# Kernel tuning notes

Hardware: AMD Instinct MI355X
Metric: run time of the kernel (lower is better)

## Reference

```python
import jax, jax.numpy as jnp
import numpy as np

HIDDEN = 128
AUG = 2          # aug_dim
SUBSTEPS = 2     # fixed dopri5 substeps per output interval (replaces adaptive stepping)
B = 16384
T = 8


def _xavier(key, shape, gain=5.0 / 3.0):
    fan_in, fan_out = shape
    lim = gain * np.sqrt(6.0 / (fan_in + fan_out))
    return jax.random.uniform(key, shape, jnp.float32, -lim, lim)


def setup_inputs() -> dict:
    key = jax.random.key(0)
    ks = jax.random.split(key, 4)
    return {
        "r0": jax.random.normal(ks[0], (B, 2), jnp.float32),
        "t": jnp.linspace(0.0, 1.0, T, dtype=jnp.float32),
        "W1": _xavier(ks[1], (5, HIDDEN)),
        "b1": jnp.zeros((HIDDEN,), jnp.float32),
        "W2": _xavier(ks[2], (HIDDEN, HIDDEN)),
        "b2": jnp.zeros((HIDDEN,), jnp.float32),
        "W3": _xavier(ks[3], (HIDDEN, 2)),
        "b3": jnp.zeros((2,), jnp.float32),
    }


def _ode_f(t, s, W1, b1, W2, b2, W3, b3):
    # s: [B, 2+AUG]; t: scalar -> concat time feature, tiny tanh MLP
    tf = t * jnp.ones((s.shape[0], 1), s.dtype)
    inp = jnp.concatenate([s, tf], axis=-1)            # [B, 5]
    h = jnp.tanh(inp @ W1 + b1)                        # [B, 128]
    h = jnp.tanh(h @ W2 + b2)                          # [B, 128]
    v_xy = h @ W3 + b3                                 # [B, 2]
    v_a = jnp.zeros((s.shape[0], AUG), s.dtype)        # static aug dynamics
    return jnp.concatenate([v_xy, v_a], axis=-1)


def _dopri5_step(f, t, s, dt):
    # Dormand-Prince RK45 tableau, 5th-order solution advance (as torchdiffeq dopri5)
    k1 = f(t, s)
    k2 = f(t + dt * (1.0 / 5.0), s + dt * (1.0 / 5.0) * k1)
    k3 = f(t + dt * (3.0 / 10.0), s + dt * ((3.0 / 40.0) * k1 + (9.0 / 40.0) * k2))
    k4 = f(t + dt * (4.0 / 5.0),
           s + dt * ((44.0 / 45.0) * k1 - (56.0 / 15.0) * k2 + (32.0 / 9.0) * k3))
    k5 = f(t + dt * (8.0 / 9.0),
           s + dt * ((19372.0 / 6561.0) * k1 - (25360.0 / 2187.0) * k2
                     + (64448.0 / 6561.0) * k3 - (212.0 / 729.0) * k4))
    k6 = f(t + dt,
           s + dt * ((9017.0 / 3168.0) * k1 - (355.0 / 33.0) * k2
                     + (46732.0 / 5247.0) * k3 + (49.0 / 176.0) * k4
                     - (5103.0 / 18656.0) * k5))
    return s + dt * ((35.0 / 384.0) * k1 + (500.0 / 1113.0) * k3
                     + (125.0 / 192.0) * k4 - (2187.0 / 6784.0) * k5
                     + (11.0 / 84.0) * k6)


def _integrate(r0, t, W1, b1, W2, b2, W3, b3):
    s0 = jnp.concatenate([r0, jnp.zeros((r0.shape[0], AUG), r0.dtype)], axis=-1)
    f = lambda tt, ss: _ode_f(tt, ss, W1, b1, W2, b2, W3, b3)

    def interval(s, ts):
        t0, t1 = ts
        dt = (t1 - t0) / SUBSTEPS
        for j in range(SUBSTEPS):  # small fixed loop, unrolled
            s = _dopri5_step(f, t0 + j * dt, s, dt)
        return s, s

    _, ys = jax.lax.scan(interval, s0, (t[:-1], t[1:]))   # [T-1, B, 4]
    traj = jnp.concatenate([s0[None], ys], axis=0)        # [T, B, 4]
    return jnp.transpose(traj, (1, 0, 2))[..., :2]        # [B, T, 2]


def reference(r0, t, W1, b1, W2, b2, W3, b3):
    return _integrate(r0, t, W1, b1, W2, b2, W3, b3)
```

## Files before the change

### kernel.cpp

```cpp
#include <hip/hip_runtime.h>


#define HID 128
#define NS  16
#define NWAVE 4
#define TT  8
#define F(a,b) ((float)((double)(a)/(double)(b)))

typedef __attribute__((ext_vector_type(8))) short bf16x8;
typedef __attribute__((ext_vector_type(4))) float f32x4;
typedef __attribute__((ext_vector_type(2))) float f32x2;

union Frag { bf16x8 v; unsigned short u[8]; unsigned int d[4]; };

__device__ __forceinline__ f32x2 bc(float s) { return f32x2{s, s}; }
__device__ __forceinline__ f32x2 pk_fma(f32x2 a, f32x2 b, f32x2 c) {
#if __has_builtin(__builtin_elementwise_fma)
  return __builtin_elementwise_fma(a, b, c);
#else
  return a * b + c;
#endif
}
__device__ __forceinline__ float exp2_fast(float x) {
#if __has_builtin(__builtin_amdgcn_exp2f)
  return __builtin_amdgcn_exp2f(x);
#else
  return __builtin_exp2f(x);
#endif
}

__device__ __forceinline__ unsigned short f2bf(float f) {
  unsigned u = __builtin_bit_cast(unsigned, f);
  u += 0x7FFFu + ((u >> 16) & 1u);
  return (unsigned short)(u >> 16);
}
__device__ __forceinline__ unsigned pack2bf(float a, float b) {
  unsigned ua = __builtin_bit_cast(unsigned, a);
  unsigned ub = __builtin_bit_cast(unsigned, b);
  ua += 0x7FFFu + ((ua >> 16) & 1u);
  ub += 0x7FFFu + ((ub >> 16) & 1u);
  return __builtin_amdgcn_perm(ub, ua, 0x07060302u);
}

__device__ __forceinline__ f32x2 tanh_pk(f32x2 x) {
  const float K2 = 2.8853900817779268f;
  f32x2 u = x * bc(K2);
  f32x2 e;
  e.x = exp2_fast(u.x);
  e.y = exp2_fast(u.y);
  f32x2 d = e + bc(1.0f);
  f32x2 r;
  r.x = __builtin_amdgcn_rcpf(d.x);
  r.y = __builtin_amdgcn_rcpf(d.y);
  return pk_fma(bc(-2.0f), r, bc(1.0f));
}

__global__ __launch_bounds__(256, 4) void node_kernel(
    const float* __restrict__ r0, const float* __restrict__ tarr,
    const float* __restrict__ W1, const float* __restrict__ b1,
    const float* __restrict__ W2, const float* __restrict__ b2,
    const float* __restrict__ W3, const float* __restrict__ b3,
    float* __restrict__ out)
{
  __shared__ uint4  h1L[16 * NS];
  __shared__ float2 vrS[NWAVE * NS];

  const int tid  = (int)threadIdx.x;
  const int lane = tid & 63;
  const int w    = __builtin_amdgcn_readfirstlane(tid >> 6);
  const int quad = lane >> 4;
  const int m16  = lane & 15;
  const int n    = tid & 15;
  const int r    = tid >> 4;
  const int s    = (int)blockIdx.x * NS + n;

  f32x2 w1x[4], w1y[4], w1t[4], bb1[4];
  #pragma unroll
  for (int p = 0; p < 4; ++p) {
    int i = r * 8 + 2 * p;
    w1x[p] = f32x2{W1[0 * HID + i], W1[0 * HID + i + 1]};
    w1y[p] = f32x2{W1[1 * HID + i], W1[1 * HID + i + 1]};
    w1t[p] = f32x2{W1[4 * HID + i], W1[4 * HID + i + 1]};
    bb1[p] = f32x2{b1[i], b1[i + 1]};
  }
  Frag Ah[2][4];
  #pragma unroll
  for (int oti = 0; oti < 2; ++oti) {
    int o = (2 * w + oti) * 16 + m16;
    #pragma unroll
    for (int kk = 0; kk < 4; ++kk)
      #pragma unroll
      for (int j = 0; j < 8; ++j)
        Ah[oti][kk].u[j] = f2bf(W2[(kk * 32 + quad * 8 + j) * HID + o]);
  }
  f32x2 b2p[2][2], w3xy[2][4];
  #pragma unroll
  for (int oti = 0; oti < 2; ++oti) {
    #pragma unroll
    for (int p = 0; p < 2; ++p) {
      int o = (2 * w + oti) * 16 + quad * 4 + 2 * p;
      b2p[oti][p] = f32x2{b2[o], b2[o + 1]};
    }
    #pragma unroll
    for (int rr = 0; rr < 4; ++rr) {
      int o = (2 * w + oti) * 16 + quad * 4 + rr;
      w3xy[oti][rr] = f32x2{W3[o * 2 + 0], W3[o * 2 + 1]};
    }
  }
  const f32x2 b3v = f32x2{b3[0], b3[1]};

  f32x2 S = f32x2{r0[2 * s + 0], r0[2 * s + 1]};
  if (tid < NS) *(float2*)&out[(s * TT + 0) * 2] = make_float2(S.x, S.y);

  auto feval = [&](float tt, f32x2 st) -> f32x2 {
    const f32x2 sx = bc(st.x), sy = bc(st.y), tv = bc(tt);
    {
      uint4 pk;
      unsigned pd[4];
      #pragma unroll
      for (int p = 0; p < 4; ++p) {
        f32x2 a = pk_fma(sx, w1x[p], bb1[p]);
        a = pk_fma(sy, w1y[p], a);
        a = pk_fma(tv, w1t[p], a);
        f32x2 h = tanh_pk(a);
        pd[p] = pack2bf(h.x, h.y);
      }
      pk.x = pd[0]; pk.y = pd[1]; pk.z = pd[2]; pk.w = pd[3];
      h1L[r * NS + n] = pk;
    }
    __syncthreads();
    f32x4 acc[2];
    acc[0] = f32x4{0.f, 0.f, 0.f, 0.f};
    acc[1] = f32x4{0.f, 0.f, 0.f, 0.f};
    #pragma unroll
    for (int kk = 0; kk < 4; ++kk) {
      Frag bfr;
      uint4 t4 = h1L[(kk * 4 + quad) * NS + m16];
      bfr.d[0] = t4.x; bfr.d[1] = t4.y; bfr.d[2] = t4.z; bfr.d[3] = t4.w;
      acc[0] = __builtin_amdgcn_mfma_f32_16x16x32_bf16(Ah[0][kk].v, bfr.v, acc[0], 0, 0, 0);
      acc[1] = __builtin_amdgcn_mfma_f32_16x16x32_bf16(Ah[1][kk].v, bfr.v, acc[1], 0, 0, 0);
    }
    f32x2 vsum = bc(0.f);
    #pragma unroll
    for (int oti = 0; oti < 2; ++oti) {
      #pragma unroll
      for (int p = 0; p < 2; ++p) {
        f32x2 av = f32x2{acc[oti][2 * p], acc[oti][2 * p + 1]} + b2p[oti][p];
        f32x2 h2 = tanh_pk(av);
        vsum = pk_fma(bc(h2.x), w3xy[oti][2 * p + 0], vsum);
        vsum = pk_fma(bc(h2.y), w3xy[oti][2 * p + 1], vsum);
      }
    }
    float px = vsum.x, py = vsum.y;
    px += __shfl_xor(px, 16); px += __shfl_xor(px, 32);
    py += __shfl_xor(py, 16); py += __shfl_xor(py, 32);
    if (lane < 16) vrS[w * NS + m16] = make_float2(px, py);
    __syncthreads();
    f32x2 rv = b3v;
    #pragma unroll
    for (int ww = 0; ww < NWAVE; ++ww) {
      float2 pp = vrS[ww * NS + n];
      rv += f32x2{pp.x, pp.y};
    }
    return rv;
  };

  #pragma unroll 1
  for (int iv = 0; iv < TT - 1; ++iv) {
    float t0 = tarr[iv], t1 = tarr[iv + 1];
    float dt = (t1 - t0) * 0.5f;
    #pragma unroll 1
    for (int ss = 0; ss < 2; ++ss) {
      float tb = (ss == 0) ? t0 : (t0 + dt);
      const f32x2 dtv = bc(dt);
      f32x2 k1 = feval(tb, S);
      f32x2 k2 = feval(tb + dt * F(1,5), pk_fma(bc(dt * F(1,5)), k1, S));
      f32x2 a3 = pk_fma(bc(F(9,40)), k2, bc(F(3,40)) * k1);
      f32x2 k3 = feval(tb + dt * F(3,10), pk_fma(dtv, a3, S));
      f32x2 a4 = pk_fma(bc(F(44,45)), k1,
                 pk_fma(bc(-F(56,15)), k2, bc(F(32,9)) * k3));
      f32x2 k4 = feval(tb + dt * F(4,5), pk_fma(dtv, a4, S));
      f32x2 a5 = pk_fma(bc(F(19372,6561)), k1,
                 pk_fma(bc(-F(25360,2187)), k2,
                 pk_fma(bc(F(64448,6561)), k3, bc(-F(212,729)) * k4)));
      f32x2 k5 = feval(tb + dt * F(8,9), pk_fma(dtv, a5, S));
      f32x2 a6 = pk_fma(bc(F(9017,3168)), k1,
                 pk_fma(bc(-F(355,33)), k2,
                 pk_fma(bc(F(46732,5247)), k3,
                 pk_fma(bc(F(49,176)), k4, bc(-F(5103,18656)) * k5))));
      f32x2 k6 = feval(tb + dt, pk_fma(dtv, a6, S));
      f32x2 fin = pk_fma(bc(F(35,384)), k1,
                  pk_fma(bc(F(500,1113)), k3,
                  pk_fma(bc(F(125,192)), k4,
                  pk_fma(bc(-F(2187,6784)), k5, bc(F(11,84)) * k6))));
      S = pk_fma(dtv, fin, S);
    }
    if (tid < NS) *(float2*)&out[(s * TT + iv + 1) * 2] = make_float2(S.x, S.y);
  }
}

extern "C" void kernel_launch(void* const* d_in, const int* in_sizes, int n_in,
                              void* d_out, int out_size, void* d_ws, size_t ws_size,
                              hipStream_t stream) {
  const float* r0 = (const float*)d_in[0];
  const float* t  = (const float*)d_in[1];
  const float* W1 = (const float*)d_in[2];
  const float* b1 = (const float*)d_in[3];
  const float* W2 = (const float*)d_in[4];
  const float* b2 = (const float*)d_in[5];
  const float* W3 = (const float*)d_in[6];
  const float* b3 = (const float*)d_in[7];
  float* out = (float*)d_out;
  const int B = in_sizes[0] / 2;
  dim3 grid(B / NS), block(NWAVE * 64);
  node_kernel<<<grid, block, 0, stream>>>(r0, t, W1, b1, W2, b2, W3, b3, out);
}
```

Measured before the change: 203.8 us.

## Process two sample groups per block and fold tanh scale into weights

```diff
diff --git a/kernel.cpp b/kernel.cpp
--- a/kernel.cpp
+++ b/kernel.cpp
@@ -2,7 +2,7 @@
 
 
 #define HID 128
-#define NS  16
+#define NSG 16
 #define NWAVE 4
 #define TT  8
 #define F(a,b) ((float)((double)(a)/(double)(b)))
@@ -28,7 +28,6 @@
   return __builtin_exp2f(x);
 #endif
 }
-
 __device__ __forceinline__ unsigned short f2bf(float f) {
   unsigned u = __builtin_bit_cast(unsigned, f);
   u += 0x7FFFu + ((u >> 16) & 1u);
@@ -41,10 +40,7 @@
   ub += 0x7FFFu + ((ub >> 16) & 1u);
   return __builtin_amdgcn_perm(ub, ua, 0x07060302u);
 }
-
-__device__ __forceinline__ f32x2 tanh_pk(f32x2 x) {
-  const float K2 = 2.8853900817779268f;
-  f32x2 u = x * bc(K2);
+__device__ __forceinline__ f32x2 tanh_pre(f32x2 u) {
   f32x2 e;
   e.x = exp2_fast(u.x);
   e.y = exp2_fast(u.y);
@@ -55,15 +51,17 @@
   return pk_fma(bc(-2.0f), r, bc(1.0f));
 }
 
-__global__ __launch_bounds__(256, 4) void node_kernel(
+#define K2C 2.8853900817779268f
+
+__global__ __launch_bounds__(256, 2) void node_kernel(
     const float* __restrict__ r0, const float* __restrict__ tarr,
     const float* __restrict__ W1, const float* __restrict__ b1,
     const float* __restrict__ W2, const float* __restrict__ b2,
     const float* __restrict__ W3, const float* __restrict__ b3,
     float* __restrict__ out)
 {
-  __shared__ uint4  h1L[16 * NS];
-  __shared__ float2 vrS[NWAVE * NS];
+  __shared__ uint4  h1L[2][16 * NSG];
+  __shared__ float2 vrS[2][NWAVE * NSG];
 
   const int tid  = (int)threadIdx.x;
   const int lane = tid & 63;
@@ -72,16 +70,17 @@
   const int m16  = lane & 15;
   const int n    = tid & 15;
   const int r    = tid >> 4;
-  const int s    = (int)blockIdx.x * NS + n;
+  const int sA   = (int)blockIdx.x * (2 * NSG) + n;
+  const int sB   = sA + NSG;
 
   f32x2 w1x[4], w1y[4], w1t[4], bb1[4];
   #pragma unroll
   for (int p = 0; p < 4; ++p) {
     int i = r * 8 + 2 * p;
-    w1x[p] = f32x2{W1[0 * HID + i], W1[0 * HID + i + 1]};
-    w1y[p] = f32x2{W1[1 * HID + i], W1[1 * HID + i + 1]};
-    w1t[p] = f32x2{W1[4 * HID + i], W1[4 * HID + i + 1]};
-    bb1[p] = f32x2{b1[i], b1[i + 1]};
+    w1x[p] = f32x2{W1[0 * HID + i], W1[0 * HID + i + 1]} * bc(K2C);
+    w1y[p] = f32x2{W1[1 * HID + i], W1[1 * HID + i + 1]} * bc(K2C);
+    w1t[p] = f32x2{W1[4 * HID + i], W1[4 * HID + i + 1]} * bc(K2C);
+    bb1[p] = f32x2{b1[i], b1[i + 1]} * bc(K2C);
   }
   Frag Ah[2][4];
   #pragma unroll
@@ -91,7 +90,7 @@
     for (int kk = 0; kk < 4; ++kk)
       #pragma unroll
       for (int j = 0; j < 8; ++j)
-        Ah[oti][kk].u[j] = f2bf(W2[(kk * 32 + quad * 8 + j) * HID + o]);
+        Ah[oti][kk].u[j] = f2bf(W2[(kk * 32 + quad * 8 + j) * HID + o] * K2C);
   }
   f32x2 b2p[2][2], w3xy[2][4];
   #pragma unroll
@@ -99,7 +98,7 @@
     #pragma unroll
     for (int p = 0; p < 2; ++p) {
       int o = (2 * w + oti) * 16 + quad * 4 + 2 * p;
-      b2p[oti][p] = f32x2{b2[o], b2[o + 1]};
+      b2p[oti][p] = f32x2{b2[o], b2[o + 1]} * bc(K2C);
     }
     #pragma unroll
     for (int rr = 0; rr < 4; ++rr) {
@@ -109,60 +108,92 @@
   }
   const f32x2 b3v = f32x2{b3[0], b3[1]};
 
-  f32x2 S = f32x2{r0[2 * s + 0], r0[2 * s + 1]};
-  if (tid < NS) *(float2*)&out[(s * TT + 0) * 2] = make_float2(S.x, S.y);
-
-  auto feval = [&](float tt, f32x2 st) -> f32x2 {
+  f32x2 SA = f32x2{r0[2 * sA + 0], r0[2 * sA + 1]};
+  f32x2 SB = f32x2{r0[2 * sB + 0], r0[2 * sB + 1]};
+  if (tid < 32) {
+    int g = tid >> 4;
+    int ss = (int)blockIdx.x * (2 * NSG) + tid;
+    f32x2 S0 = g ? SB : SA;
+    *(float2*)&out[(ss * TT + 0) * 2] = make_float2(S0.x, S0.y);
+  }
+
+  auto layer1 = [&](int g, f32x2 st, float tt) {
     const f32x2 sx = bc(st.x), sy = bc(st.y), tv = bc(tt);
-    {
-      uint4 pk;
-      unsigned pd[4];
-      #pragma unroll
-      for (int p = 0; p < 4; ++p) {
-        f32x2 a = pk_fma(sx, w1x[p], bb1[p]);
-        a = pk_fma(sy, w1y[p], a);
-        a = pk_fma(tv, w1t[p], a);
-        f32x2 h = tanh_pk(a);
-        pd[p] = pack2bf(h.x, h.y);
-      }
-      pk.x = pd[0]; pk.y = pd[1]; pk.z = pd[2]; pk.w = pd[3];
-      h1L[r * NS + n] = pk;
-    }
+    unsigned pd[4];
+    #pragma unroll
+    for (int p = 0; p < 4; ++p) {
+      f32x2 a = pk_fma(sx, w1x[p], bb1[p]);
+      a = pk_fma(sy, w1y[p], a);
+      a = pk_fma(tv, w1t[p], a);
+      f32x2 h = tanh_pre(a);
+      pd[p] = pack2bf(h.x, h.y);
+    }
+    h1L[g][r * NSG + n] = make_uint4(pd[0], pd[1], pd[2], pd[3]);
+  };
+
+  auto feval2 = [&](float tt, f32x2 stA, f32x2 stB, f32x2& vA, f32x2& vB) {
+    layer1(0, stA, tt);
+    layer1(1, stB, tt);
     __syncthreads();
-    f32x4 acc[2];
-    acc[0] = f32x4{0.f, 0.f, 0.f, 0.f};
-    acc[1] = f32x4{0.f, 0.f, 0.f, 0.f};
+    Frag bfA[4], bfB[4];
     #pragma unroll
     for (int kk = 0; kk < 4; ++kk) {
-      Frag bfr;
-      uint4 t4 = h1L[(kk * 4 + quad) * NS + m16];
-      bfr.d[0] = t4.x; bfr.d[1] = t4.y; bfr.d[2] = t4.z; bfr.d[3] = t4.w;
-      acc[0] = __builtin_amdgcn_mfma_f32_16x16x32_bf16(Ah[0][kk].v, bfr.v, acc[0], 0, 0, 0);
-      acc[1] = __builtin_amdgcn_mfma_f32_16x16x32_bf16(Ah[1][kk].v, bfr.v, acc[1], 0, 0, 0);
-    }
-    f32x2 vsum = bc(0.f);
-    #pragma unroll
-    for (int oti = 0; oti < 2; ++oti) {
+      uint4 ta = h1L[0][(kk * 4 + quad) * NSG + m16];
+      bfA[kk].d[0] = ta.x; bfA[kk].d[1] = ta.y; bfA[kk].d[2] = ta.z; bfA[kk].d[3] = ta.w;
+      uint4 tb = h1L[1][(kk * 4 + quad) * NSG + m16];
+      bfB[kk].d[0] = tb.x; bfB[kk].d[1] = tb.y; bfB[kk].d[2] = tb.z; bfB[kk].d[3] = tb.w;
+    }
+    f32x4 accA[2], accB[2];
+    accA[0] = f32x4{0.f,0.f,0.f,0.f}; accA[1] = f32x4{0.f,0.f,0.f,0.f};
+    accB[0] = f32x4{0.f,0.f,0.f,0.f}; accB[1] = f32x4{0.f,0.f,0.f,0.f};
+    #pragma unroll
+    for (int kk = 0; kk < 4; ++kk) {
+      accA[0] = __builtin_amdgcn_mfma_f32_16x16x32_bf16(Ah[0][kk].v, bfA[kk].v, accA[0], 0, 0, 0);
+      accA[1] = __builtin_amdgcn_mfma_f32_16x16x32_bf16(Ah[1][kk].v, bfA[kk].v, accA[1], 0, 0, 0);
+    }
+    #pragma unroll
+    for (int kk = 0; kk < 4; ++kk) {
+      accB[0] = __builtin_amdgcn_mfma_f32_16x16x32_bf16(Ah[0][kk].v, bfB[kk].v, accB[0], 0, 0, 0);
+      accB[1] = __builtin_amdgcn_mfma_f32_16x16x32_bf16(Ah[1][kk].v, bfB[kk].v, accB[1], 0, 0, 0);
+    }
+    f32x2 vsA = bc(0.f), vsB = bc(0.f);
+    #pragma unroll
+    for (int oti = 0; oti < 2; ++oti)
       #pragma unroll
       for (int p = 0; p < 2; ++p) {
-        f32x2 av = f32x2{acc[oti][2 * p], acc[oti][2 * p + 1]} + b2p[oti][p];
-        f32x2 h2 = tanh_pk(av);
-        vsum = pk_fma(bc(h2.x), w3xy[oti][2 * p + 0], vsum);
-        vsum = pk_fma(bc(h2.y), w3xy[oti][2 * p + 1], vsum);
-      }
-    }
-    float px = vsum.x, py = vsum.y;
-    px += __shfl_xor(px, 16); px += __shfl_xor(px, 32);
-    py += __shfl_xor(py, 16); py += __shfl_xor(py, 32);
-    if (lane < 16) vrS[w * NS + m16] = make_float2(px, py);
+        f32x2 av = f32x2{accA[oti][2*p], accA[oti][2*p+1]} + b2p[oti][p];
+        f32x2 h2 = tanh_pre(av);
+        vsA = pk_fma(bc(h2.x), w3xy[oti][2*p+0], vsA);
+        vsA = pk_fma(bc(h2.y), w3xy[oti][2*p+1], vsA);
+      }
+    #pragma unroll
+    for (int oti = 0; oti < 2; ++oti)
+      #pragma unroll
+      for (int p = 0; p < 2; ++p) {
+        f32x2 av = f32x2{accB[oti][2*p], accB[oti][2*p+1]} + b2p[oti][p];
+        f32x2 h2 = tanh_pre(av);
+        vsB = pk_fma(bc(h2.x), w3xy[oti][2*p+0], vsB);
+        vsB = pk_fma(bc(h2.y), w3xy[oti][2*p+1], vsB);
+      }
+    float pxA = vsA.x, pyA = vsA.y, pxB = vsB.x, pyB = vsB.y;
+    pxA += __shfl_xor(pxA, 16); pxA += __shfl_xor(pxA, 32);
+    pyA += __shfl_xor(pyA, 16); pyA += __shfl_xor(pyA, 32);
+    pxB += __shfl_xor(pxB, 16); pxB += __shfl_xor(pxB, 32);
+    pyB += __shfl_xor(pyB, 16); pyB += __shfl_xor(pyB, 32);
+    if (lane < 16) {
+      vrS[0][w * NSG + m16] = make_float2(pxA, pyA);
+      vrS[1][w * NSG + m16] = make_float2(pxB, pyB);
+    }
     __syncthreads();
-    f32x2 rv = b3v;
+    f32x2 ra = b3v, rb = b3v;
     #pragma unroll
     for (int ww = 0; ww < NWAVE; ++ww) {
-      float2 pp = vrS[ww * NS + n];
-      rv += f32x2{pp.x, pp.y};
-    }
-    return rv;
+      float2 pa = vrS[0][ww * NSG + n];
+      float2 pb = vrS[1][ww * NSG + n];
+      ra += f32x2{pa.x, pa.y};
+      rb += f32x2{pb.x, pb.y};
+    }
+    vA = ra; vB = rb;
   };
 
   #pragma unroll 1
@@ -173,29 +204,53 @@
     for (int ss = 0; ss < 2; ++ss) {
       float tb = (ss == 0) ? t0 : (t0 + dt);
       const f32x2 dtv = bc(dt);
-      f32x2 k1 = feval(tb, S);
-      f32x2 k2 = feval(tb + dt * F(1,5), pk_fma(bc(dt * F(1,5)), k1, S));
-      f32x2 a3 = pk_fma(bc(F(9,40)), k2, bc(F(3,40)) * k1);
-      f32x2 k3 = feval(tb + dt * F(3,10), pk_fma(dtv, a3, S));
-      f32x2 a4 = pk_fma(bc(F(44,45)), k1,
-                 pk_fma(bc(-F(56,15)), k2, bc(F(32,9)) * k3));
-      f32x2 k4 = feval(tb + dt * F(4,5), pk_fma(dtv, a4, S));
-      f32x2 a5 = pk_fma(bc(F(19372,6561)), k1,
-                 pk_fma(bc(-F(25360,2187)), k2,
-                 pk_fma(bc(F(64448,6561)), k3, bc(-F(212,729)) * k4)));
-      f32x2 k5 = feval(tb + dt * F(8,9), pk_fma(dtv, a5, S));
-      f32x2 a6 = pk_fma(bc(F(9017,3168)), k1,
-                 pk_fma(bc(-F(355,33)), k2,
-                 pk_fma(bc(F(46732,5247)), k3,
-                 pk_fma(bc(F(49,176)), k4, bc(-F(5103,18656)) * k5))));
-      f32x2 k6 = feval(tb + dt, pk_fma(dtv, a6, S));
-      f32x2 fin = pk_fma(bc(F(35,384)), k1,
-                  pk_fma(bc(F(500,1113)), k3,
-                  pk_fma(bc(F(125,192)), k4,
-                  pk_fma(bc(-F(2187,6784)), k5, bc(F(11,84)) * k6))));
-      S = pk_fma(dtv, fin, S);
-    }
-    if (tid < NS) *(float2*)&out[(s * TT + iv + 1) * 2] = make_float2(S.x, S.y);
+      f32x2 k1A, k1B, k2A, k2B, k3A, k3B, k4A, k4B, k5A, k5B, k6A, k6B;
+      feval2(tb, SA, SB, k1A, k1B);
+      { f32x2 c = bc(dt * F(1,5));
+        feval2(tb + dt * F(1,5), pk_fma(c, k1A, SA), pk_fma(c, k1B, SB), k2A, k2B); }
+      {
+        f32x2 aA = pk_fma(bc(F(9,40)), k2A, bc(F(3,40)) * k1A);
+        f32x2 aB = pk_fma(bc(F(9,40)), k2B, bc(F(3,40)) * k1B);
+        feval2(tb + dt * F(3,10), pk_fma(dtv, aA, SA), pk_fma(dtv, aB, SB), k3A, k3B);
+      }
+      {
+        f32x2 aA = pk_fma(bc(F(44,45)), k1A, pk_fma(bc(-F(56,15)), k2A, bc(F(32,9)) * k3A));
+        f32x2 aB = pk_fma(bc(F(44,45)), k1B, pk_fma(bc(-F(56,15)), k2B, bc(F(32,9)) * k3B));
+        feval2(tb + dt * F(4,5), pk_fma(dtv, aA, SA), pk_fma(dtv, aB, SB), k4A, k4B);
+      }
+      {
+        f32x2 aA = pk_fma(bc(F(19372,6561)), k1A, pk_fma(bc(-F(25360,2187)), k2A,
+                   pk_fma(bc(F(64448,6561)), k3A, bc(-F(212,729)) * k4A)));
+        f32x2 aB = pk_fma(bc(F(19372,6561)), k1B, pk_fma(bc(-F(25360,2187)), k2B,
+                   pk_fma(bc(F(64448,6561)), k3B, bc(-F(212,729)) * k4B)));
+        feval2(tb + dt * F(8,9), pk_fma(dtv, aA, SA), pk_fma(dtv, aB, SB), k5A, k5B);
+      }
+      {
+        f32x2 aA = pk_fma(bc(F(9017,3168)), k1A, pk_fma(bc(-F(355,33)), k2A,
+                   pk_fma(bc(F(46732,5247)), k3A, pk_fma(bc(F(49,176)), k4A,
+                   bc(-F(5103,18656)) * k5A))));
+        f32x2 aB = pk_fma(bc(F(9017,3168)), k1B, pk_fma(bc(-F(355,33)), k2B,
+                   pk_fma(bc(F(46732,5247)), k3B, pk_fma(bc(F(49,176)), k4B,
+                   bc(-F(5103,18656)) * k5B))));
+        feval2(tb + dt, pk_fma(dtv, aA, SA), pk_fma(dtv, aB, SB), k6A, k6B);
+      }
+      {
+        f32x2 fA = pk_fma(bc(F(35,384)), k1A, pk_fma(bc(F(500,1113)), k3A,
+                   pk_fma(bc(F(125,192)), k4A, pk_fma(bc(-F(2187,6784)), k5A,
+                   bc(F(11,84)) * k6A))));
+        f32x2 fB = pk_fma(bc(F(35,384)), k1B, pk_fma(bc(F(500,1113)), k3B,
+                   pk_fma(bc(F(125,192)), k4B, pk_fma(bc(-F(2187,6784)), k5B,
+                   bc(F(11,84)) * k6B))));
+        SA = pk_fma(dtv, fA, SA);
+        SB = pk_fma(dtv, fB, SB);
+      }
+    }
+    if (tid < 32) {
+      int g = tid >> 4;
+      int ss = (int)blockIdx.x * (2 * NSG) + tid;
+      f32x2 Sg = g ? SB : SA;
+      *(float2*)&out[(ss * TT + iv + 1) * 2] = make_float2(Sg.x, Sg.y);
+    }
   }
 }
 
@@ -212,6 +267,6 @@
   const float* b3 = (const float*)d_in[7];
   float* out = (float*)d_out;
   const int B = in_sizes[0] / 2;
-  dim3 grid(B / NS), block(NWAVE * 64);
+  dim3 grid(B / (2 * NSG)), block(NWAVE * 64);
   node_kernel<<<grid, block, 0, stream>>>(r0, t, W1, b1, W2, b2, W3, b3, out);
 }
```

Result: faster. 199.2 us (-2.3%).

## Use single-wave blocks to drop LDS exchange and barriers per feval

Applied to the files above, without the earlier changes.

```diff
diff --git a/kernel.cpp b/kernel.cpp
--- a/kernel.cpp
+++ b/kernel.cpp
@@ -2,10 +2,9 @@
 
 
 #define HID 128
-#define NS  16
-#define NWAVE 4
 #define TT  8
 #define F(a,b) ((float)((double)(a)/(double)(b)))
+#define K2C 2.8853900817779268f
 
 typedef __attribute__((ext_vector_type(8))) short bf16x8;
 typedef __attribute__((ext_vector_type(4))) float f32x4;
@@ -28,7 +27,6 @@
   return __builtin_exp2f(x);
 #endif
 }
-
 __device__ __forceinline__ unsigned short f2bf(float f) {
   unsigned u = __builtin_bit_cast(unsigned, f);
   u += 0x7FFFu + ((u >> 16) & 1u);
@@ -41,10 +39,7 @@
   ub += 0x7FFFu + ((ub >> 16) & 1u);
   return __builtin_amdgcn_perm(ub, ua, 0x07060302u);
 }
-
-__device__ __forceinline__ f32x2 tanh_pk(f32x2 x) {
-  const float K2 = 2.8853900817779268f;
-  f32x2 u = x * bc(K2);
+__device__ __forceinline__ f32x2 tanh_pre(f32x2 u) {
   f32x2 e;
   e.x = exp2_fast(u.x);
   e.y = exp2_fast(u.y);
@@ -55,114 +50,92 @@
   return pk_fma(bc(-2.0f), r, bc(1.0f));
 }
 
-__global__ __launch_bounds__(256, 4) void node_kernel(
+__global__ __launch_bounds__(64, 1) void node_kernel(
     const float* __restrict__ r0, const float* __restrict__ tarr,
     const float* __restrict__ W1, const float* __restrict__ b1,
     const float* __restrict__ W2, const float* __restrict__ b2,
     const float* __restrict__ W3, const float* __restrict__ b3,
     float* __restrict__ out)
 {
-  __shared__ uint4  h1L[16 * NS];
-  __shared__ float2 vrS[NWAVE * NS];
-
-  const int tid  = (int)threadIdx.x;
-  const int lane = tid & 63;
-  const int w    = __builtin_amdgcn_readfirstlane(tid >> 6);
+  const int lane = (int)(threadIdx.x & 63u);
   const int quad = lane >> 4;
   const int m16  = lane & 15;
-  const int n    = tid & 15;
-  const int r    = tid >> 4;
-  const int s    = (int)blockIdx.x * NS + n;
+  const int s    = (int)blockIdx.x * 16 + m16;
 
-  f32x2 w1x[4], w1y[4], w1t[4], bb1[4];
+  f32x2 w1x[16], w1y[16], w1t[16], bb1[16];
   #pragma unroll
-  for (int p = 0; p < 4; ++p) {
-    int i = r * 8 + 2 * p;
-    w1x[p] = f32x2{W1[0 * HID + i], W1[0 * HID + i + 1]};
-    w1y[p] = f32x2{W1[1 * HID + i], W1[1 * HID + i + 1]};
-    w1t[p] = f32x2{W1[4 * HID + i], W1[4 * HID + i + 1]};
-    bb1[p] = f32x2{b1[i], b1[i + 1]};
-  }
-  Frag Ah[2][4];
+  for (int kk = 0; kk < 4; ++kk)
+    #pragma unroll
+    for (int p = 0; p < 4; ++p) {
+      int i = kk * 32 + quad * 8 + 2 * p;
+      int idx = kk * 4 + p;
+      w1x[idx] = f32x2{W1[0 * HID + i], W1[0 * HID + i + 1]} * bc(K2C);
+      w1y[idx] = f32x2{W1[1 * HID + i], W1[1 * HID + i + 1]} * bc(K2C);
+      w1t[idx] = f32x2{W1[4 * HID + i], W1[4 * HID + i + 1]} * bc(K2C);
+      bb1[idx] = f32x2{b1[i], b1[i + 1]} * bc(K2C);
+    }
+  Frag W2f[8][4];
   #pragma unroll
-  for (int oti = 0; oti < 2; ++oti) {
-    int o = (2 * w + oti) * 16 + m16;
+  for (int t = 0; t < 8; ++t) {
+    int o = t * 16 + m16;
     #pragma unroll
     for (int kk = 0; kk < 4; ++kk)
       #pragma unroll
       for (int j = 0; j < 8; ++j)
-        Ah[oti][kk].u[j] = f2bf(W2[(kk * 32 + quad * 8 + j) * HID + o]);
+        W2f[t][kk].u[j] = f2bf(W2[(kk * 32 + quad * 8 + j) * HID + o] * K2C);
   }
-  f32x2 b2p[2][2], w3xy[2][4];
+  f32x4 b2i[8];
+  f32x2 w3v[8][4];
   #pragma unroll
-  for (int oti = 0; oti < 2; ++oti) {
-    #pragma unroll
-    for (int p = 0; p < 2; ++p) {
-      int o = (2 * w + oti) * 16 + quad * 4 + 2 * p;
-      b2p[oti][p] = f32x2{b2[o], b2[o + 1]};
-    }
+  for (int t = 0; t < 8; ++t)
     #pragma unroll
     for (int rr = 0; rr < 4; ++rr) {
-      int o = (2 * w + oti) * 16 + quad * 4 + rr;
-      w3xy[oti][rr] = f32x2{W3[o * 2 + 0], W3[o * 2 + 1]};
+      int o = t * 16 + quad * 4 + rr;
+      b2i[t][rr] = b2[o] * K2C;
+      w3v[t][rr] = f32x2{W3[o * 2 + 0], W3[o * 2 + 1]};
     }
-  }
   const f32x2 b3v = f32x2{b3[0], b3[1]};
 
   f32x2 S = f32x2{r0[2 * s + 0], r0[2 * s + 1]};
-  if (tid < NS) *(float2*)&out[(s * TT + 0) * 2] = make_float2(S.x, S.y);
+  if (lane < 16) *(float2*)&out[(s * TT + 0) * 2] = make_float2(S.x, S.y);
 
   auto feval = [&](float tt, f32x2 st) -> f32x2 {
     const f32x2 sx = bc(st.x), sy = bc(st.y), tv = bc(tt);
-    {
-      uint4 pk;
-      unsigned pd[4];
-      #pragma unroll
-      for (int p = 0; p < 4; ++p) {
-        f32x2 a = pk_fma(sx, w1x[p], bb1[p]);
-        a = pk_fma(sy, w1y[p], a);
-        a = pk_fma(tv, w1t[p], a);
-        f32x2 h = tanh_pk(a);
-        pd[p] = pack2bf(h.x, h.y);
-      }
-      pk.x = pd[0]; pk.y = pd[1]; pk.z = pd[2]; pk.w = pd[3];
-      h1L[r * NS + n] = pk;
+    unsigned hd[16];
+    #pragma unroll
+    for (int idx = 0; idx < 16; ++idx) {
+      f32x2 a = pk_fma(sx, w1x[idx], bb1[idx]);
+      a = pk_fma(sy, w1y[idx], a);
+      a = pk_fma(tv, w1t[idx], a);
+      f32x2 h = tanh_pre(a);
+      hd[idx] = pack2bf(h.x, h.y);
     }
-    __syncthreads();
-    f32x4 acc[2];
-    acc[0] = f32x4{0.f, 0.f, 0.f, 0.f};
-    acc[1] = f32x4{0.f, 0.f, 0.f, 0.f};
+    f32x4 acc[8];
+    #pragma unroll
+    for (int t = 0; t < 8; ++t) acc[t] = b2i[t];
     #pragma unroll
     for (int kk = 0; kk < 4; ++kk) {
-      Frag bfr;
-      uint4 t4 = h1L[(kk * 4 + quad) * NS + m16];
-      bfr.d[0] = t4.x; bfr.d[1] = t4.y; bfr.d[2] = t4.z; bfr.d[3] = t4.w;
-      acc[0] = __builtin_amdgcn_mfma_f32_16x16x32_bf16(Ah[0][kk].v, bfr.v, acc[0], 0, 0, 0);
-      acc[1] = __builtin_amdgcn_mfma_f32_16x16x32_bf16(Ah[1][kk].v, bfr.v, acc[1], 0, 0, 0);
+      Frag bv;
+      bv.d[0] = hd[kk * 4 + 0]; bv.d[1] = hd[kk * 4 + 1];
+      bv.d[2] = hd[kk * 4 + 2]; bv.d[3] = hd[kk * 4 + 3];
+      #pragma unroll
+      for (int t = 0; t < 8; ++t)
+        acc[t] = __builtin_amdgcn_mfma_f32_16x16x32_bf16(W2f[t][kk].v, bv.v, acc[t], 0, 0, 0);
     }
-    f32x2 vsum = bc(0.f);
+    f32x2 vs = bc(0.f);
     #pragma unroll
-    for (int oti = 0; oti < 2; ++oti) {
+    for (int t = 0; t < 8; ++t)
       #pragma unroll
       for (int p = 0; p < 2; ++p) {
-        f32x2 av = f32x2{acc[oti][2 * p], acc[oti][2 * p + 1]} + b2p[oti][p];
-        f32x2 h2 = tanh_pk(av);
-        vsum = pk_fma(bc(h2.x), w3xy[oti][2 * p + 0], vsum);
-        vsum = pk_fma(bc(h2.y), w3xy[oti][2 * p + 1], vsum);
+        f32x2 av = f32x2{acc[t][2 * p], acc[t][2 * p + 1]};
+        f32x2 h2 = tanh_pre(av);
+        vs = pk_fma(bc(h2.x), w3v[t][2 * p + 0], vs);
+        vs = pk_fma(bc(h2.y), w3v[t][2 * p + 1], vs);
       }
-    }
-    float px = vsum.x, py = vsum.y;
+    float px = vs.x, py = vs.y;
     px += __shfl_xor(px, 16); px += __shfl_xor(px, 32);
     py += __shfl_xor(py, 16); py += __shfl_xor(py, 32);
-    if (lane < 16) vrS[w * NS + m16] = make_float2(px, py);
-    __syncthreads();
-    f32x2 rv = b3v;
-    #pragma unroll
-    for (int ww = 0; ww < NWAVE; ++ww) {
-      float2 pp = vrS[ww * NS + n];
-      rv += f32x2{pp.x, pp.y};
-    }
-    return rv;
+    return f32x2{px, py} + b3v;
   };
 
   #pragma unroll 1
@@ -195,7 +168,7 @@
                   pk_fma(bc(-F(2187,6784)), k5, bc(F(11,84)) * k6))));
       S = pk_fma(dtv, fin, S);
     }
-    if (tid < NS) *(float2*)&out[(s * TT + iv + 1) * 2] = make_float2(S.x, S.y);
+    if (lane < 16) *(float2*)&out[(s * TT + iv + 1) * 2] = make_float2(S.x, S.y);
   }
 }
 
@@ -212,6 +185,6 @@
   const float* b3 = (const float*)d_in[7];
   float* out = (float*)d_out;
   const int B = in_sizes[0] / 2;
-  dim3 grid(B / NS), block(NWAVE * 64);
+  dim3 grid(B / 16), block(64);
   node_kernel<<<grid, block, 0, stream>>>(r0, t, W1, b1, W2, b2, W3, b3, out);
 }
```

Measured after the change: 195.5 us. 4.1% less time.
